# Kernel optimization log

Measured on AMD Instinct MI355X. Metric: run time of the kernel, lower is better.

The kernel has to match this reference:

```python
import jax, jax.numpy as jnp
import numpy as np

N = 200_000   # points
C = 20        # semantic classes
P = 256       # proposals (from bfs_cluster)
M = 400_000   # (proposal, point) pairs
CLUSTER_PROPOSE_POINTS = 100
VOXEL_SIZE = 0.02


def setup_inputs() -> dict:
    key = jax.random.key(0)
    k1, k2, k3, k4, k5 = jax.random.split(key, 5)
    return {
        "logit_pred": jax.random.normal(k1, (N, C), jnp.float32),
        "bias_pred": jax.random.normal(k2, (N, 3), jnp.float32),
        "coord": jax.random.normal(k3, (N, 3), jnp.float32) * 5.0,
        "proposal_ids": jax.random.randint(k4, (M,), 0, P, dtype=jnp.int32),
        "point_ids": jax.random.randint(k5, (M,), 0, N, dtype=jnp.int32),
    }


def reference(logit_pred, bias_pred, coord, proposal_ids, point_ids):
    # voxelized predicted instance centers (center_pred /= voxel_size)
    center_pred = (coord + bias_pred) / VOXEL_SIZE

    # softmax + argmax semantic prediction
    probs = jax.nn.softmax(logit_pred, axis=-1)          # [N, C]
    segment_pred = jnp.argmax(probs, axis=1)             # [N]

    # dense proposal mask construction (scatter): proposals_pred[pid, point] = 1
    proposals_pred = jnp.zeros((P, N), jnp.int32).at[proposal_ids, point_ids].set(1)
    counts = proposals_pred.sum(axis=1)                  # [P]
    proposals_mask = counts > CLUSTER_PROPOSE_POINTS     # [P] keep mask

    # instance class = semantic class of the representative (first) point per proposal
    rep = jax.ops.segment_min(point_ids, proposal_ids, num_segments=P)  # [P]
    instance_pred = segment_pred[jnp.clip(rep, 0, N - 1)]               # [P]

    # per-proposal mean confidence: mean over proposal points of probs[point, cls]
    conf = probs[:, instance_pred]                       # [N, P] gather of class columns
    score_sum = jnp.einsum("pn,np->p", proposals_pred.astype(probs.dtype), conf)
    pred_scores = jnp.where(proposals_mask,
                            score_sum / jnp.maximum(counts, 1).astype(probs.dtype),
                            0.0)                         # [P]

    # filtered masks/classes (kept at fixed shape; invalid rows zeroed / class -1)
    pred_masks = proposals_pred * proposals_mask[:, None].astype(jnp.int32)
    pred_classes = jnp.where(proposals_mask, instance_pred, -1)

    return pred_scores, pred_masks, pred_classes, bias_pred, probs
```

## Files before the change

### kernel.cpp

```cpp
#include <hip/hip_runtime.h>

static constexpr int    kN = 200000;
static constexpr int    kC = 20;
static constexpr int    kP = 256;
static constexpr int    kM = 400000;
static constexpr int    kThreshPts = 100;
static constexpr int    kRowCap = 2048;
static constexpr int    kLWords = kN / 32;

typedef float nfloat4 __attribute__((ext_vector_type(4)));

static constexpr size_t OFF_SCORES  = 0;
static constexpr size_t OFF_MASKS   = 256;
static constexpr size_t OFF_CLASSES = OFF_MASKS + (size_t)kP * kN;
static constexpr size_t OFF_BIAS    = OFF_CLASSES + 256;
static constexpr size_t OFF_PROBS   = OFF_BIAS + 3 * (size_t)kN;

static constexpr size_t WS_CURSOR = 0;
static constexpr size_t WS_SEG    = 1024;
static constexpr size_t WS_ROWBUF = WS_SEG + (size_t)kN * 4;

static constexpr int kBucketBlocks = (kM / 4 + 255) / 256;
static constexpr int kSoftBlocks   = (kN + 255) / 256;

__global__ void k_front(const float* __restrict__ logit,
                        const float* __restrict__ bias,
                        const int4* __restrict__ prop4,
                        const int4* __restrict__ pt4,
                        int* __restrict__ cursor,
                        int* __restrict__ rowbuf,
                        int* __restrict__ seg,
                        float* __restrict__ out) {
    int t = threadIdx.x;

    if (blockIdx.x < kBucketBlocks) {
        __shared__ int s_cnt[kP];
        __shared__ int s_off[kP];
        s_cnt[t] = 0;
        __syncthreads();

        int idx = blockIdx.x * 256 + t;
        bool valid = idx < (kM / 4);
        int4 pv = {0, 0, 0, 0}, nv = {0, 0, 0, 0};
        int sl[4] = {0, 0, 0, 0};
        if (valid) {
            pv = prop4[idx];
            nv = pt4[idx];
            sl[0] = atomicAdd(&s_cnt[pv.x], 1);
            sl[1] = atomicAdd(&s_cnt[pv.y], 1);
            sl[2] = atomicAdd(&s_cnt[pv.z], 1);
            sl[3] = atomicAdd(&s_cnt[pv.w], 1);
        }
        __syncthreads();
        s_off[t] = s_cnt[t] ? atomicAdd(&cursor[t], s_cnt[t]) : 0;
        __syncthreads();
        if (valid) {
            int d0 = s_off[pv.x] + sl[0];
            int d1 = s_off[pv.y] + sl[1];
            int d2 = s_off[pv.z] + sl[2];
            int d3 = s_off[pv.w] + sl[3];
            if (d0 < kRowCap) rowbuf[pv.x * kRowCap + d0] = nv.x;
            if (d1 < kRowCap) rowbuf[pv.y * kRowCap + d1] = nv.y;
            if (d2 < kRowCap) rowbuf[pv.z * kRowCap + d2] = nv.z;
            if (d3 < kRowCap) rowbuf[pv.w * kRowCap + d3] = nv.w;
        }
        return;
    }

    int tid = (blockIdx.x - kBucketBlocks) * 256 + t;

    if (tid < 150000) {
        const float4* b4 = (const float4*)bias;
        float4*       o4 = (float4*)(out + OFF_BIAS);
        o4[tid] = b4[tid];
    }
    if (tid >= kN) return;

    const float4* l4 = (const float4*)(logit + (size_t)tid * kC);
    float v[kC];
#pragma unroll
    for (int c = 0; c < 5; c++) {
        float4 x = l4[c];
        v[4*c] = x.x; v[4*c+1] = x.y; v[4*c+2] = x.z; v[4*c+3] = x.w;
    }
    float m = v[0]; int arg = 0;
#pragma unroll
    for (int i = 1; i < kC; i++) if (v[i] > m) { m = v[i]; arg = i; }
    float s = 0.0f;
#pragma unroll
    for (int i = 0; i < kC; i++) { v[i] = __expf(v[i] - m); s += v[i]; }
    float inv = 1.0f / s;
    float4* p4 = (float4*)(out + OFF_PROBS + (size_t)tid * kC);
#pragma unroll
    for (int c = 0; c < 5; c++) {
        float4 x;
        x.x = v[4*c] * inv; x.y = v[4*c+1] * inv;
        x.z = v[4*c+2] * inv; x.w = v[4*c+3] * inv;
        p4[c] = x;
    }
    seg[tid] = arg;
}

__global__ void __launch_bounds__(1024)
k_row(const int* __restrict__ rowbuf,
      const int* __restrict__ cursor,
      const int* __restrict__ seg,
      float* __restrict__ out) {
    __shared__ unsigned int lbits[kLWords];
    __shared__ int   s_redc[16];
    __shared__ int   s_redm[16];
    __shared__ float s_redf[16];
    __shared__ int   s_cls;
    __shared__ float s_fv;

    int p = blockIdx.x;
    int t = threadIdx.x;
    const float* probs = out + OFF_PROBS;

    for (int i = t; i < kLWords; i += 1024) lbits[i] = 0;
    int len = cursor[p];
    if (len > kRowCap) len = kRowCap;
    __syncthreads();

    const int* rb = rowbuf + p * kRowCap;
    int  n0 = 0, n1 = 0;
    bool u0 = false, u1 = false;
    int  mymin = 0x7fffffff;
    if (t < len) {
        n0 = rb[t];
        unsigned int bit = 1u << (n0 & 31);
        unsigned int old = atomicOr(&lbits[(unsigned)n0 >> 5], bit);
        u0 = (old & bit) == 0u;
        mymin = n0;
    }
    if (t + 1024 < len) {
        n1 = rb[t + 1024];
        unsigned int bit = 1u << (n1 & 31);
        unsigned int old = atomicOr(&lbits[(unsigned)n1 >> 5], bit);
        u1 = (old & bit) == 0u;
        mymin = n1 < mymin ? n1 : mymin;
    }

    int cnt = (int)u0 + (int)u1;
    for (int off = 32; off; off >>= 1) {
        cnt += __shfl_down(cnt, off);
        int om = __shfl_down(mymin, off);
        mymin = om < mymin ? om : mymin;
    }
    if ((t & 63) == 0) { s_redc[t >> 6] = cnt; s_redm[t >> 6] = mymin; }
    __syncthreads();
    int tot = 0;
    if (t == 0) {
        int mn = 0x7fffffff;
        for (int i = 0; i < 16; i++) {
            tot += s_redc[i];
            mn = s_redm[i] < mn ? s_redm[i] : mn;
        }
        int r = mn < 0 ? 0 : (mn > kN - 1 ? kN - 1 : mn);
        int c = seg[r];
        bool fl = tot > kThreshPts;
        s_cls = c;
        s_fv  = fl ? 1.0f : 0.0f;
        out[OFF_CLASSES + p] = fl ? (float)c : -1.0f;
    }
    __syncthreads();

    float fv = s_fv;
    int   c  = s_cls;

    float g0 = 0.0f, g1 = 0.0f;
    if (u0) g0 = probs[(size_t)n0 * kC + c];
    if (u1) g1 = probs[(size_t)n1 * kC + c];

    nfloat4* mrow = (nfloat4*)(out + OFF_MASKS) + (size_t)p * (kN / 4);
    for (int f = t; f < kN / 4; f += 1024) {
        unsigned int word = lbits[f >> 3];
        unsigned int b    = (word >> (((unsigned)f & 7u) * 4u)) & 0xFu;
        nfloat4 o;
        o.x = (b & 1u) ? fv : 0.0f;
        o.y = (b & 2u) ? fv : 0.0f;
        o.z = (b & 4u) ? fv : 0.0f;
        o.w = (b & 8u) ? fv : 0.0f;
        mrow[f] = o;
    }

    float s = g0 + g1;
    for (int off = 32; off; off >>= 1) s += __shfl_down(s, off);
    if ((t & 63) == 0) s_redf[t >> 6] = s;
    __syncthreads();
    if (t == 0) {
        float stot = 0.0f;
        for (int i = 0; i < 16; i++) stot += s_redf[i];
        float denom = (float)(tot > 1 ? tot : 1);
        out[OFF_SCORES + p] = (s_fv != 0.0f) ? stot / denom : 0.0f;
    }
}

extern "C" void kernel_launch(void* const* d_in, const int* in_sizes, int n_in,
                              void* d_out, int out_size, void* d_ws, size_t ws_size,
                              hipStream_t stream) {
    const float* logit = (const float*)d_in[0];
    const float* bias  = (const float*)d_in[1];
    const int4* prop4 = (const int4*)d_in[3];
    const int4* pt4   = (const int4*)d_in[4];
    float* out = (float*)d_out;
    char*  ws  = (char*)d_ws;

    int* cursor = (int*)(ws + WS_CURSOR);
    int* seg    = (int*)(ws + WS_SEG);
    int* rowbuf = (int*)(ws + WS_ROWBUF);

    hipMemsetAsync(cursor, 0, kP * sizeof(int), stream);
    k_front<<<kBucketBlocks + kSoftBlocks, 256, 0, stream>>>(
        logit, bias, prop4, pt4, cursor, rowbuf, seg, out);
    k_row<<<kP, 1024, 0, stream>>>(rowbuf, cursor, seg, out);
}
```

Baseline: 256.1 us.

## Fuse front and row kernels into one persistent kernel with grid barrier

Merges the softmax/bucketing kernel and the per-proposal row kernel into a single 256-block, 1024-thread launch, separated by a software grid barrier built on an atomic counter in the workspace. Each block handles one slice of the softmax, the bias copy and a chunk of the pair bucketing, then waits at the barrier before building its proposal's mask row. This removes one kernel launch and the gap between the two kernels. In exchange, the front phase now runs on only 256 blocks of 1024 threads instead of many small blocks. Correctness depends on all 256 blocks being resident at once so the spin barrier cannot deadlock.

After: 307.5 us. +20.1%, slower.

```diff
diff --git a/kernel.cpp b/kernel.cpp
--- a/kernel.cpp
+++ b/kernel.cpp
@@ -7,6 +7,9 @@
 static constexpr int    kThreshPts = 100;
 static constexpr int    kRowCap = 2048;
 static constexpr int    kLWords = kN / 32;
+static constexpr int    kBlocks = 256;
+static constexpr int    kThreads = 1024;
+static constexpr int    kChunk4 = (kM / 4 + kBlocks - 1) / kBlocks;
 
 typedef float nfloat4 __attribute__((ext_vector_type(4)));
 
@@ -17,95 +20,22 @@
 static constexpr size_t OFF_PROBS   = OFF_BIAS + 3 * (size_t)kN;
 
 static constexpr size_t WS_CURSOR = 0;
-static constexpr size_t WS_SEG    = 1024;
+static constexpr size_t WS_BAR    = 1024;
+static constexpr size_t WS_SEG    = 1152;
 static constexpr size_t WS_ROWBUF = WS_SEG + (size_t)kN * 4;
 
-static constexpr int kBucketBlocks = (kM / 4 + 255) / 256;
-static constexpr int kSoftBlocks   = (kN + 255) / 256;
-
-__global__ void k_front(const float* __restrict__ logit,
-                        const float* __restrict__ bias,
-                        const int4* __restrict__ prop4,
-                        const int4* __restrict__ pt4,
-                        int* __restrict__ cursor,
-                        int* __restrict__ rowbuf,
-                        int* __restrict__ seg,
-                        float* __restrict__ out) {
-    int t = threadIdx.x;
-
-    if (blockIdx.x < kBucketBlocks) {
-        __shared__ int s_cnt[kP];
-        __shared__ int s_off[kP];
-        s_cnt[t] = 0;
-        __syncthreads();
-
-        int idx = blockIdx.x * 256 + t;
-        bool valid = idx < (kM / 4);
-        int4 pv = {0, 0, 0, 0}, nv = {0, 0, 0, 0};
-        int sl[4] = {0, 0, 0, 0};
-        if (valid) {
-            pv = prop4[idx];
-            nv = pt4[idx];
-            sl[0] = atomicAdd(&s_cnt[pv.x], 1);
-            sl[1] = atomicAdd(&s_cnt[pv.y], 1);
-            sl[2] = atomicAdd(&s_cnt[pv.z], 1);
-            sl[3] = atomicAdd(&s_cnt[pv.w], 1);
-        }
-        __syncthreads();
-        s_off[t] = s_cnt[t] ? atomicAdd(&cursor[t], s_cnt[t]) : 0;
-        __syncthreads();
-        if (valid) {
-            int d0 = s_off[pv.x] + sl[0];
-            int d1 = s_off[pv.y] + sl[1];
-            int d2 = s_off[pv.z] + sl[2];
-            int d3 = s_off[pv.w] + sl[3];
-            if (d0 < kRowCap) rowbuf[pv.x * kRowCap + d0] = nv.x;
-            if (d1 < kRowCap) rowbuf[pv.y * kRowCap + d1] = nv.y;
-            if (d2 < kRowCap) rowbuf[pv.z * kRowCap + d2] = nv.z;
-            if (d3 < kRowCap) rowbuf[pv.w * kRowCap + d3] = nv.w;
-        }
-        return;
-    }
-
-    int tid = (blockIdx.x - kBucketBlocks) * 256 + t;
-
-    if (tid < 150000) {
-        const float4* b4 = (const float4*)bias;
-        float4*       o4 = (float4*)(out + OFF_BIAS);
-        o4[tid] = b4[tid];
-    }
-    if (tid >= kN) return;
-
-    const float4* l4 = (const float4*)(logit + (size_t)tid * kC);
-    float v[kC];
-#pragma unroll
-    for (int c = 0; c < 5; c++) {
-        float4 x = l4[c];
-        v[4*c] = x.x; v[4*c+1] = x.y; v[4*c+2] = x.z; v[4*c+3] = x.w;
-    }
-    float m = v[0]; int arg = 0;
-#pragma unroll
-    for (int i = 1; i < kC; i++) if (v[i] > m) { m = v[i]; arg = i; }
-    float s = 0.0f;
-#pragma unroll
-    for (int i = 0; i < kC; i++) { v[i] = __expf(v[i] - m); s += v[i]; }
-    float inv = 1.0f / s;
-    float4* p4 = (float4*)(out + OFF_PROBS + (size_t)tid * kC);
-#pragma unroll
-    for (int c = 0; c < 5; c++) {
-        float4 x;
-        x.x = v[4*c] * inv; x.y = v[4*c+1] * inv;
-        x.z = v[4*c+2] * inv; x.w = v[4*c+3] * inv;
-        p4[c] = x;
-    }
-    seg[tid] = arg;
-}
-
 __global__ void __launch_bounds__(1024)
-k_row(const int* __restrict__ rowbuf,
-      const int* __restrict__ cursor,
-      const int* __restrict__ seg,
-      float* __restrict__ out) {
+k_fused(const float* __restrict__ logit,
+        const float* __restrict__ bias,
+        const int4* __restrict__ prop4,
+        const int4* __restrict__ pt4,
+        int* __restrict__ cursor,
+        int* __restrict__ bar,
+        int* __restrict__ rowbuf,
+        int* __restrict__ seg,
+        float* __restrict__ out) {
+    __shared__ int s_cnt[kP];
+    __shared__ int s_off[kP];
     __shared__ unsigned int lbits[kLWords];
     __shared__ int   s_redc[16];
     __shared__ int   s_redm[16];
@@ -113,11 +43,87 @@
     __shared__ int   s_cls;
     __shared__ float s_fv;
 
-    int p = blockIdx.x;
-    int t = threadIdx.x;
+    const int t = threadIdx.x;
+    const int b = blockIdx.x;
+    const int gtid = b * kThreads + t;
+
+    if (gtid < 150000) {
+        const float4* b4 = (const float4*)bias;
+        float4*       o4 = (float4*)(out + OFF_BIAS);
+        o4[gtid] = b4[gtid];
+    }
+    if (gtid < kN) {
+        const float4* l4 = (const float4*)(logit + (size_t)gtid * kC);
+        float v[kC];
+#pragma unroll
+        for (int c = 0; c < 5; c++) {
+            float4 x = l4[c];
+            v[4*c] = x.x; v[4*c+1] = x.y; v[4*c+2] = x.z; v[4*c+3] = x.w;
+        }
+        float m = v[0]; int arg = 0;
+#pragma unroll
+        for (int i = 1; i < kC; i++) if (v[i] > m) { m = v[i]; arg = i; }
+        float s = 0.0f;
+#pragma unroll
+        for (int i = 0; i < kC; i++) { v[i] = __expf(v[i] - m); s += v[i]; }
+        float inv = 1.0f / s;
+        float4* p4 = (float4*)(out + OFF_PROBS + (size_t)gtid * kC);
+#pragma unroll
+        for (int c = 0; c < 5; c++) {
+            float4 x;
+            x.x = v[4*c] * inv; x.y = v[4*c+1] * inv;
+            x.z = v[4*c+2] * inv; x.w = v[4*c+3] * inv;
+            p4[c] = x;
+        }
+        seg[gtid] = arg;
+    }
+
+    if (t < kP) s_cnt[t] = 0;
+    __syncthreads();
+
+    int idx = b * kChunk4 + t;
+    bool valid = (t < kChunk4) && (idx < kM / 4);
+    int4 pv = {0, 0, 0, 0}, nv = {0, 0, 0, 0};
+    int sl[4] = {0, 0, 0, 0};
+    if (valid) {
+        pv = prop4[idx];
+        nv = pt4[idx];
+        sl[0] = atomicAdd(&s_cnt[pv.x], 1);
+        sl[1] = atomicAdd(&s_cnt[pv.y], 1);
+        sl[2] = atomicAdd(&s_cnt[pv.z], 1);
+        sl[3] = atomicAdd(&s_cnt[pv.w], 1);
+    }
+    __syncthreads();
+    if (t < kP) s_off[t] = s_cnt[t] ? atomicAdd(&cursor[t], s_cnt[t]) : 0;
+    __syncthreads();
+    if (valid) {
+        int d0 = s_off[pv.x] + sl[0];
+        int d1 = s_off[pv.y] + sl[1];
+        int d2 = s_off[pv.z] + sl[2];
+        int d3 = s_off[pv.w] + sl[3];
+        if (d0 < kRowCap) rowbuf[pv.x * kRowCap + d0] = nv.x;
+        if (d1 < kRowCap) rowbuf[pv.y * kRowCap + d1] = nv.y;
+        if (d2 < kRowCap) rowbuf[pv.z * kRowCap + d2] = nv.z;
+        if (d3 < kRowCap) rowbuf[pv.w * kRowCap + d3] = nv.w;
+    }
+
+    __syncthreads();
+    if (t == 0) {
+        int arrived = __hip_atomic_fetch_add(bar, 1, __ATOMIC_ACQ_REL,
+                                             __HIP_MEMORY_SCOPE_AGENT);
+        if (arrived + 1 < kBlocks) {
+            while (__hip_atomic_load(bar, __ATOMIC_ACQUIRE,
+                                     __HIP_MEMORY_SCOPE_AGENT) < kBlocks) {
+                __builtin_amdgcn_s_sleep(2);
+            }
+        }
+    }
+    __syncthreads();
+
+    const int p = b;
     const float* probs = out + OFF_PROBS;
 
-    for (int i = t; i < kLWords; i += 1024) lbits[i] = 0;
+    for (int i = t; i < kLWords; i += kThreads) lbits[i] = 0;
     int len = cursor[p];
     if (len > kRowCap) len = kRowCap;
     __syncthreads();
@@ -133,8 +139,8 @@
         u0 = (old & bit) == 0u;
         mymin = n0;
     }
-    if (t + 1024 < len) {
-        n1 = rb[t + 1024];
+    if (t + kThreads < len) {
+        n1 = rb[t + kThreads];
         unsigned int bit = 1u << (n1 & 31);
         unsigned int old = atomicOr(&lbits[(unsigned)n1 >> 5], bit);
         u1 = (old & bit) == 0u;
@@ -173,14 +179,14 @@
     if (u1) g1 = probs[(size_t)n1 * kC + c];
 
     nfloat4* mrow = (nfloat4*)(out + OFF_MASKS) + (size_t)p * (kN / 4);
-    for (int f = t; f < kN / 4; f += 1024) {
+    for (int f = t; f < kN / 4; f += kThreads) {
         unsigned int word = lbits[f >> 3];
-        unsigned int b    = (word >> (((unsigned)f & 7u) * 4u)) & 0xFu;
+        unsigned int bb   = (word >> (((unsigned)f & 7u) * 4u)) & 0xFu;
         nfloat4 o;
-        o.x = (b & 1u) ? fv : 0.0f;
-        o.y = (b & 2u) ? fv : 0.0f;
-        o.z = (b & 4u) ? fv : 0.0f;
-        o.w = (b & 8u) ? fv : 0.0f;
+        o.x = (bb & 1u) ? fv : 0.0f;
+        o.y = (bb & 2u) ? fv : 0.0f;
+        o.z = (bb & 4u) ? fv : 0.0f;
+        o.w = (bb & 8u) ? fv : 0.0f;
         mrow[f] = o;
     }
 
@@ -207,11 +213,11 @@
     char*  ws  = (char*)d_ws;
 
     int* cursor = (int*)(ws + WS_CURSOR);
+    int* bar    = (int*)(ws + WS_BAR);
     int* seg    = (int*)(ws + WS_SEG);
     int* rowbuf = (int*)(ws + WS_ROWBUF);
 
-    hipMemsetAsync(cursor, 0, kP * sizeof(int), stream);
-    k_front<<<kBucketBlocks + kSoftBlocks, 256, 0, stream>>>(
-        logit, bias, prop4, pt4, cursor, rowbuf, seg, out);
-    k_row<<<kP, 1024, 0, stream>>>(rowbuf, cursor, seg, out);
+    hipMemsetAsync(ws, 0, WS_BAR + sizeof(int), stream);
+    k_fused<<<kBlocks, kThreads, 0, stream>>>(
+        logit, bias, prop4, pt4, cursor, bar, rowbuf, seg, out);
 }
```
